# Kernel optimization log

Measured on AMD Instinct MI355X. Metric: run time of the kernel, lower is better.

Reference implementation:

```python
import jax, jax.numpy as jnp
import numpy as np

HEADS = 2
K_HOP = 2
RATIO = 0.8
NEG_SLOPE = 0.01


def seg_softmax(logits, seg, num_seg):
    # torch_geometric.utils.softmax: numerically stable segment softmax
    m = jax.ops.segment_max(logits, seg, num_segments=num_seg)
    e = jnp.exp(logits - m[seg])
    d = jax.ops.segment_sum(e, seg, num_segments=num_seg)
    return e / d[seg]


def _attention(key_value, query, seg, num_seg, Wk, W1, W2, W3):
    # Attention.forward with enable_BN=False; weights stored [in,out] so x@W == torch Linear
    a = key_value @ Wk
    h = jnp.concatenate([a, query, a - query, a * query], axis=-1)  # [N,4H]
    h = jax.nn.leaky_relu(h @ W1, NEG_SLOPE)
    h = jax.nn.leaky_relu(h @ W2, NEG_SLOPE)
    h = jax.nn.leaky_relu(h @ W3, NEG_SLOPE)  # [N,1]
    return seg_softmax(h[:, 0], seg, num_seg)[:, None]  # att_weights [N,1]


def setup_inputs():
    key = jax.random.key(0)
    ks = jax.random.split(key, 10)
    B, n, H, epg = 64, 64, 128, 2048
    N = B * n
    x = jax.random.normal(ks[0], (N, H), jnp.float32)
    src = jax.random.randint(ks[1], (B, epg), 0, n)
    dst = jax.random.randint(ks[2], (B, epg), 0, n)
    off = (jnp.arange(B) * n)[:, None]
    edge_index = jnp.stack([(src + off).reshape(-1), (dst + off).reshape(-1)], 0)
    edge_weight = jax.random.uniform(ks[3], (B * epg,), jnp.float32)
    target_x = jax.random.normal(ks[4], (B, H), jnp.float32)
    batch_ixs = jnp.repeat(jnp.arange(B), n)
    s = lambda i, sh: jax.random.normal(ks[i], sh, jnp.float32) / np.sqrt(sh[-2])
    # index 0=cluster_att, 1=query_att, 2=cluster_att2, 3=query_att2
    att_Wk = s(5, (4, H, H))
    att_W1 = s(6, (4, 4 * H, 2 * H))
    att_W2 = s(7, (4, 2 * H, H))
    att_W3 = s(8, (4, H, 1))
    lin_W = s(9, (HEADS, H, H))
    return dict(x=x, edge_index=edge_index, edge_weight=edge_weight, target_x=target_x,
                batch_ixs=batch_ixs, att_Wk=att_Wk, att_W1=att_W1, att_W2=att_W2,
                att_W3=att_W3, lin_W=lin_W)


def reference(x, edge_index, edge_weight, target_x, batch_ixs, att_Wk, att_W1, att_W2, att_W3, lin_W):
    N, H = x.shape
    B = target_x.shape[0]
    n = N // B
    # ---- gcn_norm with self loops (fill 1.0) ----
    loop = jnp.arange(N)
    row = jnp.concatenate([edge_index[0], loop])
    col = jnp.concatenate([edge_index[1], loop])
    w = jnp.concatenate([edge_weight, jnp.ones((N,), edge_weight.dtype)])
    deg = jax.ops.segment_sum(w, col, num_segments=N)
    dinv = jnp.where(deg > 0, jax.lax.rsqrt(jnp.maximum(deg, 1e-12)), 0.0)
    ew = dinv[row] * w * dinv[col]  # [L]
    # ---- k-hop propagation ----
    def hop(v):
        return jax.ops.segment_sum(v[row] * ew[:, None], col, num_segments=N)
    x_q = x
    for _ in range(K_HOP):
        x_q = hop(x_q)
    qt = target_x[batch_ixs]  # repeat_interleave by per-graph counts (sorted batch)
    # ---- multi-head edge attention (reuse_att_w=True, dropout=0 -> E identical per head) ----
    f1 = _attention(x, x_q, batch_ixs, B, att_Wk[0], att_W1[0], att_W2[0], att_W3[0])
    f2 = _attention(x, qt, batch_ixs, B, att_Wk[1], att_W1[1], att_W2[1], att_W3[1])
    E = jax.nn.leaky_relu(f1[col] + f2[row], NEG_SLOPE)  # [L,1]
    E = seg_softmax(E[:, 0], col, N)[:, None]
    x_c = jnp.zeros_like(x)
    E_g = jnp.zeros((row.shape[0], 1), x.dtype)
    agg = jax.ops.segment_sum(x[row] * E, col, num_segments=N)
    for h in range(HEADS):
        x_c = x_c + jax.nn.leaky_relu(x + agg @ lin_W[h], NEG_SLOPE)
        E_g = E_g + E
    x_c = x_c / HEADS
    E_g = E_g / HEADS
    # ---- second k-hop + cluster scoring ----
    x_q2 = x_c
    for _ in range(K_HOP):
        x_q2 = hop(x_q2)
    g1 = _attention(x_c, x_q2, batch_ixs, B, att_Wk[2], att_W1[2], att_W2[2], att_W3[2])
    g2 = _attention(x_c, qt, batch_ixs, B, att_Wk[3], att_W1[3], att_W2[3], att_W3[3])
    # stack over heads then mean == g1+g2 (same attention modules reused per head)
    cluster_score = seg_softmax((g1 + g2)[:, 0], batch_ixs, B)  # [N]
    # ---- per-graph topk (ratio) ----
    kk = int(np.ceil(RATIO * n))
    _, idx = jax.lax.top_k(cluster_score.reshape(B, n), kk)  # descending, matches PyG topk
    perm = (idx + (jnp.arange(B) * n)[:, None]).reshape(-1)  # [Nk]
    x_out = x[perm] * cluster_score[perm][:, None]
    batch_out = batch_ixs[perm]
    # ---- S^T A S (dense equivalent of SparseTensor triple product) ----
    A_d = jnp.zeros((N, N), x.dtype).at[row, col].add(ew)
    S_d = jnp.zeros((N, N), x.dtype).at[row, col].add(E_g[:, 0])
    S_p = S_d[:, perm]  # S[:, perm] -> [N, Nk]
    A2 = S_p.T @ (A_d @ S_p)  # [Nk, Nk]
    Nk = perm.shape[0]
    A2 = A2.at[jnp.arange(Nk), jnp.arange(Nk)].set(1.0)  # fill_diag(1.0)
    return x_out, A2, batch_out, perm
```

## Files before the change

### kernel.cpp

```cpp
#include <hip/hip_runtime.h>

#define KK 52
#define NKOUT 3328
#define NEG 0.01f

typedef __attribute__((ext_vector_type(8))) __bf16 bf16x8;
typedef __attribute__((ext_vector_type(16))) float floatx16;

__device__ __forceinline__ float lrelu(float v){ return v > 0.f ? v : NEG*v; }

#define SW(r, ko) ((r)*40 + ((ko) ^ ((((r)>>3)&3) << 3)))

__device__ __forceinline__ void split_store8(const float* vv, __bf16* P0, __bf16* P1, __bf16* P2, int addr){
  bf16x8 p1, p2, p3;
  #pragma unroll
  for (int j = 0; j < 8; j++){
    __bf16 b1 = (__bf16)vv[j];
    float r1 = vv[j] - (float)b1;
    __bf16 b2 = (__bf16)r1;
    float r2 = r1 - (float)b2;
    p1[j] = b1; p2[j] = b2; p3[j] = (__bf16)r2;
  }
  *(bf16x8*)(P0 + addr) = p1;
  *(bf16x8*)(P1 + addr) = p2;
  *(bf16x8*)(P2 + addr) = p3;
}

__device__ __forceinline__ void mfma6(const __bf16* A0, const __bf16* A1, const __bf16* A2,
                                      const __bf16* B0, const __bf16* B1, const __bf16* B2,
                                      int aoff, int boff, floatx16* acc){
  bf16x8 a1 = *(const bf16x8*)(A0 + aoff);
  bf16x8 a2 = *(const bf16x8*)(A1 + aoff);
  bf16x8 a3 = *(const bf16x8*)(A2 + aoff);
  bf16x8 b1 = *(const bf16x8*)(B0 + boff);
  bf16x8 b2 = *(const bf16x8*)(B1 + boff);
  bf16x8 b3 = *(const bf16x8*)(B2 + boff);
  floatx16 c = *acc;
  c = __builtin_amdgcn_mfma_f32_32x32x16_bf16(a1,b1,c,0,0,0);
  c = __builtin_amdgcn_mfma_f32_32x32x16_bf16(a1,b2,c,0,0,0);
  c = __builtin_amdgcn_mfma_f32_32x32x16_bf16(a2,b1,c,0,0,0);
  c = __builtin_amdgcn_mfma_f32_32x32x16_bf16(a1,b3,c,0,0,0);
  c = __builtin_amdgcn_mfma_f32_32x32x16_bf16(a3,b1,c,0,0,0);
  c = __builtin_amdgcn_mfma_f32_32x32x16_bf16(a2,b2,c,0,0,0);
  *acc = c;
}

__device__ __forceinline__ void g_gemm(const float* __restrict__ A0, int ldA,
                                       const float* __restrict__ W0, int ldW, int K,
                                       __bf16* pb, floatx16* oA, floatx16* oB){
  __bf16 *As0 = pb, *As1 = pb+2560, *As2 = pb+5120;
  __bf16 *Bs0 = pb+7680, *Bs1 = pb+12800, *Bs2 = pb+17920;
  int tid = threadIdx.x;
  int sar = tid >> 2, sako = (tid & 3)*8;
  int bn = tid & 127, bk = (tid >> 7)*16;
  int wv_ = tid >> 6, L = tid & 63, m = L & 31, half = L >> 5;
  int rA = 32*(wv_ & 1) + m, rB0 = (wv_ >> 1)*32 + m, rB1 = rB0 + 64;
  const float* arow = A0 + (size_t)sar*ldA;
  floatx16 accA, accB;
  #pragma unroll
  for (int i = 0; i < 16; i++){ accA[i] = 0.f; accB[i] = 0.f; }
  float ra[8], wv[16];
  {
    float4 v0 = *(const float4*)(arow + sako);
    float4 v1 = *(const float4*)(arow + sako + 4);
    ra[0]=v0.x; ra[1]=v0.y; ra[2]=v0.z; ra[3]=v0.w; ra[4]=v1.x; ra[5]=v1.y; ra[6]=v1.z; ra[7]=v1.w;
    #pragma unroll
    for (int j = 0; j < 16; j++) wv[j] = W0[(size_t)(bk + j)*ldW + bn];
  }
  for (int k0 = 0; k0 < K; k0 += 32){
    split_store8(ra, As0, As1, As2, SW(sar, sako));
    split_store8(wv,     Bs0, Bs1, Bs2, SW(bn, bk));
    split_store8(wv + 8, Bs0, Bs1, Bs2, SW(bn, bk + 8));
    __syncthreads();
    int k1 = k0 + 32;
    float ra2[8], wv2[16];
    if (k1 < K){
      float4 v0 = *(const float4*)(arow + k1 + sako);
      float4 v1 = *(const float4*)(arow + k1 + sako + 4);
      ra2[0]=v0.x; ra2[1]=v0.y; ra2[2]=v0.z; ra2[3]=v0.w; ra2[4]=v1.x; ra2[5]=v1.y; ra2[6]=v1.z; ra2[7]=v1.w;
      #pragma unroll
      for (int j = 0; j < 16; j++) wv2[j] = W0[(size_t)(k1 + bk + j)*ldW + bn];
    }
    #pragma unroll
    for (int kg = 0; kg < 2; kg++){
      int ko = kg*16 + half*8;
      mfma6(As0,As1,As2, Bs0,Bs1,Bs2, SW(rA,ko), SW(rB0,ko), &accA);
      mfma6(As0,As1,As2, Bs0,Bs1,Bs2, SW(rA,ko), SW(rB1,ko), &accB);
    }
    __syncthreads();
    if (k1 < K){
      #pragma unroll
      for (int j = 0; j < 8; j++) ra[j] = ra2[j];
      #pragma unroll
      for (int j = 0; j < 16; j++) wv[j] = wv2[j];
    }
  }
  *oA = accA; *oB = accB;
}

__device__ __forceinline__ void g_gemm_h64(const float* __restrict__ arow, const float* __restrict__ qrow,
                                           const float* __restrict__ W1fz, int colbase,
                                           __bf16* pb, floatx16* oC){
  __bf16 *As0 = pb, *As1 = pb+2560, *As2 = pb+5120;
  __bf16 *Bs0 = pb+7680, *Bs1 = pb+10240, *Bs2 = pb+12800;
  int tid = threadIdx.x;
  int sar = tid >> 2, sako = (tid & 3)*8;
  int bn = tid & 63, bk = (tid >> 6)*8;
  int col = colbase + bn;
  int wv_ = tid >> 6, L = tid & 63, m = L & 31, half = L >> 5;
  int rA = 32*(wv_ & 1) + m, rB = 32*(wv_ >> 1) + m;
  auto loadA = [&](int k0, float* r){
    int seg = k0 >> 7, kl = (k0 & 127) + sako;
    if (seg == 0){
      float4 a0 = *(const float4*)(arow + kl), a1 = *(const float4*)(arow + kl + 4);
      r[0]=a0.x; r[1]=a0.y; r[2]=a0.z; r[3]=a0.w; r[4]=a1.x; r[5]=a1.y; r[6]=a1.z; r[7]=a1.w;
    } else if (seg == 1){
      float4 q0 = *(const float4*)(qrow + kl), q1 = *(const float4*)(qrow + kl + 4);
      r[0]=q0.x; r[1]=q0.y; r[2]=q0.z; r[3]=q0.w; r[4]=q1.x; r[5]=q1.y; r[6]=q1.z; r[7]=q1.w;
    } else {
      float4 a0 = *(const float4*)(arow + kl), a1 = *(const float4*)(arow + kl + 4);
      float4 q0 = *(const float4*)(qrow + kl), q1 = *(const float4*)(qrow + kl + 4);
      r[0]=a0.x*q0.x; r[1]=a0.y*q0.y; r[2]=a0.z*q0.z; r[3]=a0.w*q0.w;
      r[4]=a1.x*q1.x; r[5]=a1.y*q1.y; r[6]=a1.z*q1.z; r[7]=a1.w*q1.w;
    }
  };
  auto loadB = [&](int k0, float* r){
    #pragma unroll
    for (int j = 0; j < 8; j++) r[j] = W1fz[(size_t)(k0 + bk + j)*256 + col];
  };
  floatx16 acc;
  #pragma unroll
  for (int i = 0; i < 16; i++) acc[i] = 0.f;
  float ra[8], wv[8];
  loadA(0, ra); loadB(0, wv);
  for (int k0 = 0; k0 < 384; k0 += 32){
    split_store8(ra, As0, As1, As2, SW(sar, sako));
    split_store8(wv, Bs0, Bs1, Bs2, SW(bn, bk));
    __syncthreads();
    int k1 = k0 + 32;
    float ra2[8], wv2[8];
    if (k1 < 384){ loadA(k1, ra2); loadB(k1, wv2); }
    #pragma unroll
    for (int kg = 0; kg < 2; kg++){
      int ko = kg*16 + half*8;
      mfma6(As0,As1,As2, Bs0,Bs1,Bs2, SW(rA,ko), SW(rB,ko), &acc);
    }
    __syncthreads();
    if (k1 < 384){
      #pragma unroll
      for (int j = 0; j < 8; j++){ ra[j] = ra2[j]; wv[j] = wv2[j]; }
    }
  }
  *oC = acc;
}

__device__ __forceinline__ void c_write(floatx16 accA, floatx16 accB, float* C0, int ldC, int act){
  int tid = threadIdx.x, wv_ = tid >> 6, L = tid & 63, m = L & 31, half = L >> 5;
  int rB0 = (wv_ >> 1)*32 + m, rB1 = rB0 + 64;
  int row0 = 32*(wv_ & 1) + 4*half;
  #pragma unroll
  for (int reg = 0; reg < 16; reg++){
    int row = row0 + (reg & 3) + 8*(reg >> 2);
    float va = accA[reg], vb = accB[reg];
    if (act){ va = lrelu(va); vb = lrelu(vb); }
    C0[(size_t)row*ldC + rB0] = va;
    C0[(size_t)row*ldC + rB1] = vb;
  }
}

__device__ __forceinline__ void c_write64(floatx16 acc, float* C0, int ldC, int act){
  int tid = threadIdx.x, wv_ = tid >> 6, L = tid & 63, m = L & 31, half = L >> 5;
  int col = 32*(wv_ >> 1) + m;
  int row0 = 32*(wv_ & 1) + 4*half;
  #pragma unroll
  for (int reg = 0; reg < 16; reg++){
    int row = row0 + (reg & 3) + 8*(reg >> 2);
    float v = acc[reg];
    if (act) v = lrelu(v);
    C0[(size_t)row*ldC + col] = v;
  }
}

__device__ __forceinline__ void hop2_run(const float* A, const float* VfullL,
                                         const float* srcG, float* dstG,
                                         float* Vt, float* Tt){
  int tid = threadIdx.x;
  int tc = (tid & 31)*2, tf = (tid >> 5)*4;
  for (int f0 = 0; f0 < 128; f0 += 32){
    if (!VfullL){
      for (int o = tid; o < 2048; o += 256){
        int r = o >> 5, f = o & 31;
        Vt[o] = srcG[r*128 + f0 + f];
      }
      __syncthreads();
    }
    float a00,a01,a02,a03,a10,a11,a12,a13;
    a00=a01=a02=a03=a10=a11=a12=a13=0.f;
    for (int r = 0; r < 64; r++){
      float x0 = A[r*64 + tc], x1 = A[r*64 + tc + 1];
      float4 v4 = VfullL ? *(const float4*)&VfullL[r*128 + f0 + tf]
                         : *(const float4*)&Vt[r*32 + tf];
      a00 += x0*v4.x; a01 += x0*v4.y; a02 += x0*v4.z; a03 += x0*v4.w;
      a10 += x1*v4.x; a11 += x1*v4.y; a12 += x1*v4.z; a13 += x1*v4.w;
    }
    *(float4*)&Tt[tc*32 + tf]     = make_float4(a00,a01,a02,a03);
    *(float4*)&Tt[(tc+1)*32 + tf] = make_float4(a10,a11,a12,a13);
    __syncthreads();
    a00=a01=a02=a03=a10=a11=a12=a13=0.f;
    for (int r = 0; r < 64; r++){
      float x0 = A[r*64 + tc], x1 = A[r*64 + tc + 1];
      float4 v4 = *(const float4*)&Tt[r*32 + tf];
      a00 += x0*v4.x; a01 += x0*v4.y; a02 += x0*v4.z; a03 += x0*v4.w;
      a10 += x1*v4.x; a11 += x1*v4.y; a12 += x1*v4.z; a13 += x1*v4.w;
    }
    *(float4*)(dstG + tc*128 + f0 + tf)     = make_float4(a00,a01,a02,a03);
    *(float4*)(dstG + (tc+1)*128 + f0 + tf) = make_float4(a10,a11,a12,a13);
    __syncthreads();
  }
}

__global__ __launch_bounds__(256) void k_p0(const int* __restrict__ ei, const float* __restrict__ ew,
                                            const float* __restrict__ x, const float* __restrict__ Wk,
                                            const float* __restrict__ W1,
                                            float* A_g, float* M_g, float* xq, float* a_buf, float* W1f){
  __shared__ __align__(16) char POOL[57856];
  float* pf = (float*)POOL;
  __bf16* pb = (__bf16*)POOL;
  int blk = blockIdx.x, tid = threadIdx.x;
  if (blk < 64){
    int b = blk;
    float* Ws = pf; float* Mc = pf + 4096; float* dv = pf + 8192;
    for (int i = tid; i < 4096; i += 256){ Ws[i] = 0.f; Mc[i] = 0.f; }
    __syncthreads();
    const int* r0 = ei + b*2048;
    const int* c0 = ei + 64*2048 + b*2048;
    const float* w0 = ew + b*2048;
    int base = b*64;
    for (int e = tid; e < 2048; e += 256){
      int r = r0[e] - base, c = c0[e] - base;
      atomicAdd(&Ws[r*64 + c], w0[e]);
      atomicAdd(&Mc[r*64 + c], 1.f);
    }
    if (tid < 64){ atomicAdd(&Ws[tid*65], 1.f); atomicAdd(&Mc[tid*65], 1.f); }
    __syncthreads();
    if (tid < 64){
      float d = 0.f;
      for (int r = 0; r < 64; r++) d += Ws[r*64 + tid];
      dv[tid] = d > 0.f ? rsqrtf(fmaxf(d, 1e-12f)) : 0.f;
    }
    __syncthreads();
    for (int i = tid; i < 4096; i += 256){
      int r = i >> 6, c = i & 63;
      float a = dv[r]*Ws[i]*dv[c];
      Ws[i] = a;
      A_g[b*4096 + i] = a;
      M_g[b*4096 + i] = Mc[i];
    }
    __syncthreads();
    hop2_run(Ws, nullptr, x + (size_t)b*8192, xq + (size_t)b*8192, pf + 8256, pf + 10304);
  } else if (blk < 192){
    int idx = blk - 64, z = idx >> 6, b = idx & 63;
    floatx16 cA, cB;
    g_gemm(x + (size_t)b*8192, 128, Wk + (size_t)z*16384, 128, 128, pb, &cA, &cB);
    c_write(cA, cB, a_buf + (size_t)z*524288 + (size_t)b*8192, 128, 0);
  } else {
    int idx0 = (blk - 192)*6144;
    for (int i = tid; i < 6144; i += 256){
      int g = idx0 + i;
      int zz = g / 98304;
      int r = g - zz*98304;
      int kr = r >> 8, c = r & 255;
      const float* Wz = W1 + (size_t)zz*131072;
      float v;
      if (kr < 128)       v = Wz[kr*256 + c] + Wz[(kr + 256)*256 + c];
      else if (kr < 256)  v = Wz[kr*256 + c] - Wz[(kr + 128)*256 + c];
      else                v = Wz[(kr + 128)*256 + c];
      W1f[g] = v;
    }
  }
}

__global__ __launch_bounds__(256) void k_h1(const float* __restrict__ a_buf, const float* __restrict__ q0,
                                            const float* __restrict__ tgt, const float* __restrict__ W1fp,
                                            float* h1){
  __shared__ __align__(16) char POOL[30720];
  __bf16* pb = (__bf16*)POOL;
  int blk = blockIdx.x, tid = threadIdx.x;
  int b = blk >> 3, z = (blk >> 2) & 1, nq = blk & 3;
  int sar = tid >> 2;
  const float* arow = a_buf + (size_t)z*524288 + ((size_t)b*64 + sar)*128;
  const float* qrow = z ? (tgt + (size_t)b*128) : (q0 + ((size_t)b*64 + sar)*128);
  floatx16 c;
  g_gemm_h64(arow, qrow, W1fp + (size_t)z*98304, nq*64, pb, &c);
  c_write64(c, h1 + (size_t)z*1048576 + (size_t)b*16384 + nq*64, 256, 1);
}

__global__ __launch_bounds__(256) void k_w2(const float* __restrict__ h1, const float* __restrict__ W2,
                                            const float* __restrict__ W3, float* outF){
  __shared__ __align__(16) char POOL[46720];
  float* pf = (float*)POOL;
  __bf16* pb = (__bf16*)POOL;
  int blk = blockIdx.x, tid = threadIdx.x;
  int z = blk >> 6, b = blk & 63;
  const float* W2z = W2 + (size_t)z*32768;
  const float* W3z = W3 + z*128;
  floatx16 cA, cB;
  g_gemm(h1 + (size_t)z*1048576 + (size_t)b*64*256, 256, W2z, 128, 256, pb, &cA, &cB);
  int wv_ = tid >> 6, L = tid & 63, m = L & 31, half = L >> 5;
  int rB0 = (wv_ >> 1)*32 + m, rB1 = rB0 + 64;
  float wA = W3z[rB0], wB = W3z[rB1];
  float* lgp = pf + 11520;
  float c[16];
  #pragma unroll
  for (int reg = 0; reg < 16; reg++) c[reg] = lrelu(cA[reg])*wA + lrelu(cB[reg])*wB;
  #pragma unroll
  for (int off = 1; off < 32; off <<= 1)
    #pragma unroll
    for (int reg = 0; reg < 16; reg++) c[reg] += __shfl_xor(c[reg], off);
  if (m == 0){
    #pragma unroll
    for (int reg = 0; reg < 16; reg++) lgp[wv_*32 + half*16 + reg] = c[reg];
  }
  __syncthreads();
  if (tid < 64){
    int row = tid, wva = row >> 5, rem = row & 31;
    int hf = (rem >> 2) & 1, rg = (rem & 3) + 4*(rem >> 3);
    float l = lrelu(lgp[wva*32 + hf*16 + rg] + lgp[(wva + 2)*32 + hf*16 + rg]);
    float mx = l;
    #pragma unroll
    for (int off = 32; off; off >>= 1) mx = fmaxf(mx, __shfl_xor(mx, off));
    float e = expf(l - mx);
    float s = e;
    #pragma unroll
    for (int off = 32; off; off >>= 1) s += __shfl_xor(s, off);
    outF[z*4096 + b*64 + row] = e/s;
  }
}

__global__ __launch_bounds__(256) void k_edge(const float* __restrict__ M_g, const float* __restrict__ fb,
                                              const float* __restrict__ x, float* __restrict__ S_g,
                                              float* __restrict__ agg){
  __shared__ __align__(16) float Mc[4096];
  __shared__ __align__(16) float xb[8192];
  __shared__ float f1s[64], f2s[64];
  int b = blockIdx.x, tid = threadIdx.x;
  for (int i = tid; i < 4096; i += 256) Mc[i] = M_g[b*4096 + i];
  for (int i = tid*4; i < 8192; i += 1024)
    *(float4*)&xb[i] = *(const float4*)(x + (size_t)b*8192 + i);
  if (tid < 64) f1s[tid] = fb[b*64 + tid];
  else if (tid < 128) f2s[tid - 64] = fb[4096 + b*64 + (tid - 64)];
  __syncthreads();
  int c = tid >> 2, sub = tid & 3;
  float m = -1e30f;
  for (int r = sub; r < 64; r += 4)
    if (Mc[r*64 + c] > 0.f) m = fmaxf(m, lrelu(f1s[c] + f2s[r]));
  m = fmaxf(m, __shfl_xor(m, 1));
  m = fmaxf(m, __shfl_xor(m, 2));
  float s = 0.f;
  for (int r = sub; r < 64; r += 4){
    float mc = Mc[r*64 + c];
    if (mc > 0.f) s += mc*expf(lrelu(f1s[c] + f2s[r]) - m);
  }
  s += __shfl_xor(s, 1);
  s += __shfl_xor(s, 2);
  for (int r = sub; r < 64; r += 4){
    float mc = Mc[r*64 + c];
    float v = 0.f;
    if (mc > 0.f) v = mc*expf(lrelu(f1s[c] + f2s[r]) - m)/s;
    Mc[r*64 + c] = v;
  }
  __syncthreads();
  for (int i = tid; i < 4096; i += 256) S_g[b*4096 + i] = Mc[i];
  int tc = (tid & 15)*4, tf = (tid >> 4)*8;
  float acc[4][8];
  #pragma unroll
  for (int i = 0; i < 4; i++)
    #pragma unroll
    for (int j = 0; j < 8; j++) acc[i][j] = 0.f;
  for (int r = 0; r < 64; r++){
    float4 e4 = *(const float4*)&Mc[r*64 + tc];
    float4 x0 = *(const float4*)&xb[r*128 + tf];
    float4 x1 = *(const float4*)&xb[r*128 + tf + 4];
    float e_[4] = {e4.x,e4.y,e4.z,e4.w};
    float x_[8] = {x0.x,x0.y,x0.z,x0.w,x1.x,x1.y,x1.z,x1.w};
    #pragma unroll
    for (int ci = 0; ci < 4; ci++)
      #pragma unroll
      for (int fj = 0; fj < 8; fj++) acc[ci][fj] += e_[ci]*x_[fj];
  }
  #pragma unroll
  for (int ci = 0; ci < 4; ci++){
    *(float4*)(agg + (size_t)b*8192 + (tc+ci)*128 + tf)     = make_float4(acc[ci][0],acc[ci][1],acc[ci][2],acc[ci][3]);
    *(float4*)(agg + (size_t)b*8192 + (tc+ci)*128 + tf + 4) = make_float4(acc[ci][4],acc[ci][5],acc[ci][6],acc[ci][7]);
  }
}

__global__ __launch_bounds__(256) void k_linxchop(const float* __restrict__ aggb, const float* __restrict__ x,
                                                  const float* __restrict__ linW, const float* __restrict__ A_g,
                                                  float* xcb, float* xq2){
  __shared__ __align__(16) char POOL[57856];
  float* pf = (float*)POOL;
  __bf16* pb = (__bf16*)POOL;
  int b = blockIdx.x, tid = threadIdx.x;
  floatx16 h0A, h0B, h1A, h1B2;
  g_gemm(aggb + (size_t)b*8192, 128, linW, 128, 128, pb, &h0A, &h0B);
  g_gemm(aggb + (size_t)b*8192, 128, linW + 16384, 128, 128, pb, &h1A, &h1B2);
  float* xcV = pf; float* Ab = pf + 8192; float* Tt = pf + 12288;
  {
    int wv_ = tid >> 6, L = tid & 63, m = L & 31, half = L >> 5;
    int rB0 = (wv_ >> 1)*32 + m, rB1 = rB0 + 64, row0 = 32*(wv_ & 1) + 4*half;
    #pragma unroll
    for (int reg = 0; reg < 16; reg++){
      int row = row0 + (reg & 3) + 8*(reg >> 2);
      float xv0 = x[((size_t)b*64 + row)*128 + rB0];
      float v0 = 0.5f*(lrelu(xv0 + h0A[reg]) + lrelu(xv0 + h1A[reg]));
      xcV[row*128 + rB0] = v0;
      xcb[(size_t)b*8192 + row*128 + rB0] = v0;
      float xv1 = x[((size_t)b*64 + row)*128 + rB1];
      float v1 = 0.5f*(lrelu(xv1 + h0B[reg]) + lrelu(xv1 + h1B2[reg]));
      xcV[row*128 + rB1] = v1;
      xcb[(size_t)b*8192 + row*128 + rB1] = v1;
    }
  }
  for (int i = tid*4; i < 4096; i += 1024)
    *(float4*)&Ab[i] = *(const float4*)(A_g + b*4096 + i);
  __syncthreads();
  hop2_run(Ab, xcV, nullptr, xq2 + (size_t)b*8192, Tt, Tt);
}

__global__ __launch_bounds__(256) void k_wkg(const float* __restrict__ xcb, const float* __restrict__ Wkg,
                                             float* a_buf){
  __shared__ __align__(16) char POOL[46080];
  __bf16* pb = (__bf16*)POOL;
  int blk = blockIdx.x;
  int z = blk >> 6, b = blk & 63;
  floatx16 cA, cB;
  g_gemm(xcb + (size_t)b*8192, 128, Wkg + (size_t)z*16384, 128, 128, pb, &cA, &cB);
  c_write(cA, cB, a_buf + (size_t)z*524288 + (size_t)b*8192, 128, 0);
}

__global__ __launch_bounds__(256) void k_A2c(const float* __restrict__ gb, const float* __restrict__ x,
                                             const float* __restrict__ A_g, const float* __restrict__ S_g,
                                             float* C2g, float* outX, float* outB, float* outP){
  __shared__ __align__(16) float At[64*68];
  __shared__ __align__(16) float Sp[64*56];
  __shared__ __align__(16) float Tq[64*56];
  __shared__ int pi[64];
  __shared__ float pv[64];
  int b = blockIdx.x, tid = threadIdx.x;
  if (tid < 64){
    int lane = tid;
    float l = gb[b*64 + lane] + gb[4096 + b*64 + lane];
    float m = l;
    #pragma unroll
    for (int off = 32; off; off >>= 1) m = fmaxf(m, __shfl_xor(m, off));
    float e = expf(l - m);
    float sm = e;
    #pragma unroll
    for (int off = 32; off; off >>= 1) sm += __shfl_xor(sm, off);
    float v = e/sm;
    int idx = lane;
    #pragma unroll
    for (int k = 2; k <= 64; k <<= 1){
      #pragma unroll
      for (int j = k >> 1; j > 0; j >>= 1){
        float ov = __shfl_xor(v, j);
        int   oi = __shfl_xor(idx, j);
        bool ascBlock = (lane & k) == 0;
        bool iAmLow   = (lane & j) == 0;
        bool otherPrec = (ov > v) || (ov == v && oi < idx);
        bool take = (ascBlock == iAmLow) ? otherPrec : !otherPrec;
        if (take){ v = ov; idx = oi; }
      }
    }
    pi[lane] = idx; pv[lane] = v;
    if (lane < KK){
      outB[b*KK + lane] = (float)b;
      outP[b*KK + lane] = (float)(b*64 + idx);
    }
  }
  __syncthreads();
  for (int o = tid*4; o < KK*128; o += 1024){
    int j = o >> 7, f = o & 127;
    float4 xv = *(const float4*)(x + ((size_t)b*64 + pi[j])*128 + f);
    float sv = pv[j];
    *(float4*)(outX + (size_t)b*KK*128 + o) = make_float4(xv.x*sv, xv.y*sv, xv.z*sv, xv.w*sv);
  }
  for (int idx = tid; idx < 4096; idx += 256){
    int i = idx >> 6, k = idx & 63;
    At[k*68 + i] = A_g[b*4096 + idx];
  }
  for (int idx = tid; idx < 4096; idx += 256){
    int k = idx >> 6, t = idx & 63;
    if (t < 56) Sp[k*56 + t] = (t < KK) ? S_g[b*4096 + k*64 + pi[t]] : 0.f;
  }
  __syncthreads();
  if (tid < 224){
    int i0 = (tid/14)*4, t0 = (tid % 14)*4;
    float acc[4][4];
    #pragma unroll
    for (int a = 0; a < 4; a++)
      #pragma unroll
      for (int c = 0; c < 4; c++) acc[a][c] = 0.f;
    for (int k = 0; k < 64; k++){
      float4 a4 = *(const float4*)&At[k*68 + i0];
      float4 s4 = *(const float4*)&Sp[k*56 + t0];
      float a_[4] = {a4.x,a4.y,a4.z,a4.w};
      float s_[4] = {s4.x,s4.y,s4.z,s4.w};
      #pragma unroll
      for (int ii = 0; ii < 4; ii++)
        #pragma unroll
        for (int tt = 0; tt < 4; tt++) acc[ii][tt] += a_[ii]*s_[tt];
    }
    #pragma unroll
    for (int ii = 0; ii < 4; ii++)
      *(float4*)&Tq[(i0+ii)*56 + t0] = make_float4(acc[ii][0],acc[ii][1],acc[ii][2],acc[ii][3]);
  }
  __syncthreads();
  if (tid < 169){
    int a0 = (tid/13)*4, t0 = (tid % 13)*4;
    float acc[4][4];
    #pragma unroll
    for (int a = 0; a < 4; a++)
      #pragma unroll
      for (int c = 0; c < 4; c++) acc[a][c] = 0.f;
    for (int i = 0; i < 64; i++){
      float4 s4 = *(const float4*)&Sp[i*56 + a0];
      float4 t4 = *(const float4*)&Tq[i*56 + t0];
      float s_[4] = {s4.x,s4.y,s4.z,s4.w};
      float t_[4] = {t4.x,t4.y,t4.z,t4.w};
      #pragma unroll
      for (int aa = 0; aa < 4; aa++)
        #pragma unroll
        for (int tt = 0; tt < 4; tt++) acc[aa][tt] += s_[aa]*t_[tt];
    }
    #pragma unroll
    for (int aa = 0; aa < 4; aa++)
      #pragma unroll
      for (int tt = 0; tt < 4; tt++){
        int a = a0 + aa, t = t0 + tt;
        C2g[b*(KK*KK) + a*KK + t] = (a == t) ? 1.f : acc[aa][tt];
      }
  }
}

__global__ __launch_bounds__(256) void k_A2w(const float* __restrict__ C2g, float* __restrict__ outA2){
  int g = blockIdx.x*256 + threadIdx.x;
  int row = g/832, c4 = g - row*832;
  int b = row/KK, al = row - b*KK;
  int rel = c4 - b*13;
  float4 val;
  if (rel >= 0 && rel < 13){
    val = *(const float4*)(C2g + (size_t)b*(KK*KK) + al*KK + rel*4);
  } else {
    val = make_float4(0.f, 0.f, 0.f, 0.f);
  }
  *(float4*)(outA2 + (size_t)g*4) = val;
}

extern "C" void kernel_launch(void* const* d_in, const int* in_sizes, int n_in,
                              void* d_out, int out_size, void* d_ws, size_t ws_size,
                              hipStream_t stream){
  const float* x    = (const float*)d_in[0];
  const int*   ei   = (const int*)d_in[1];
  const float* ew   = (const float*)d_in[2];
  const float* tgt  = (const float*)d_in[3];
  const float* Wk   = (const float*)d_in[5];
  const float* W1   = (const float*)d_in[6];
  const float* W2   = (const float*)d_in[7];
  const float* W3   = (const float*)d_in[8];
  const float* linW = (const float*)d_in[9];
  float* out = (float*)d_out;

  float* wf   = (float*)d_ws;
  float* A_g  = wf;
  float* M_g  = wf + 262144;
  float* S_g  = wf + 524288;
  float* xq   = wf + 786432;
  float* xq2  = wf + 1310720;
  float* aggb = wf + 1835008;
  float* xcb  = wf + 2359296;
  float* a_buf= wf + 2883584;
  float* h1   = wf + 3932160;
  float* fb   = wf + 6029312;
  float* gb   = wf + 6037504;
  float* W1f  = wf + 6045696;
  float* C2g  = wf + 6438912;

  float* outX  = out;
  float* outA2 = out + 425984;
  float* outB  = out + 425984 + 11075584;
  float* outP  = outB + NKOUT;

  k_p0<<<dim3(256), dim3(256), 0, stream>>>(ei, ew, x, Wk, W1, A_g, M_g, xq, a_buf, W1f);
  k_h1<<<dim3(512), dim3(256), 0, stream>>>(a_buf, xq, tgt, W1f, h1);
  k_w2<<<dim3(128), dim3(256), 0, stream>>>(h1, W2, W3, fb);
  k_edge<<<dim3(64), dim3(256), 0, stream>>>(M_g, fb, x, S_g, aggb);
  k_linxchop<<<dim3(64), dim3(256), 0, stream>>>(aggb, x, linW, A_g, xcb, xq2);
  k_wkg<<<dim3(128), dim3(256), 0, stream>>>(xcb, Wk + 2*16384, a_buf);
  k_h1<<<dim3(512), dim3(256), 0, stream>>>(a_buf, xq2, tgt, W1f + 2*98304, h1);
  k_w2<<<dim3(128), dim3(256), 0, stream>>>(h1, W2 + 2*32768, W3 + 2*128, gb);
  k_A2c<<<dim3(64), dim3(256), 0, stream>>>(gb, x, A_g, S_g, C2g, outX, outB, outP);
  k_A2w<<<dim3(10816), dim3(256), 0, stream>>>(C2g, outA2);
}
```

Measured before the change: 257.5 us.

## Split W2/Wk GEMMs into 64-column halves, zero A2 early, write diagonal blocks directly

The W2 and Wk-gather GEMMs now use a 64-column tile variant with twice as many blocks, so more CUs are busy. The W2 stage writes partial logits per column half, and the leaky-relu plus segment softmax move into the consumer kernels. The large dense A2 output is zeroed by extra blocks appended to the first kernel, and the per-graph A2 blocks are written straight into place. This removes the separate 10816-block copy kernel and the intermediate C2 buffer, at the cost of recomputing the softmax in two consumers.

```diff
diff --git a/kernel.cpp b/kernel.cpp
--- a/kernel.cpp
+++ b/kernel.cpp
@@ -96,6 +96,55 @@
     }
   }
   *oA = accA; *oB = accB;
+}
+
+__device__ __forceinline__ void g_gemm64(const float* __restrict__ A0, int ldA,
+                                         const float* __restrict__ W0, int ldW, int K,
+                                         __bf16* pb, floatx16* oC){
+  __bf16 *As0 = pb, *As1 = pb+2560, *As2 = pb+5120;
+  __bf16 *Bs0 = pb+7680, *Bs1 = pb+10240, *Bs2 = pb+12800;
+  int tid = threadIdx.x;
+  int sar = tid >> 2, sako = (tid & 3)*8;
+  int bn = tid & 63, bk = (tid >> 6)*8;
+  int wv_ = tid >> 6, L = tid & 63, m = L & 31, half = L >> 5;
+  int rA = 32*(wv_ & 1) + m, rB = 32*(wv_ >> 1) + m;
+  const float* arow = A0 + (size_t)sar*ldA;
+  floatx16 acc;
+  #pragma unroll
+  for (int i = 0; i < 16; i++) acc[i] = 0.f;
+  float ra[8], wv[8];
+  {
+    float4 v0 = *(const float4*)(arow + sako);
+    float4 v1 = *(const float4*)(arow + sako + 4);
+    ra[0]=v0.x; ra[1]=v0.y; ra[2]=v0.z; ra[3]=v0.w; ra[4]=v1.x; ra[5]=v1.y; ra[6]=v1.z; ra[7]=v1.w;
+    #pragma unroll
+    for (int j = 0; j < 8; j++) wv[j] = W0[(size_t)(bk + j)*ldW + bn];
+  }
+  for (int k0 = 0; k0 < K; k0 += 32){
+    split_store8(ra, As0, As1, As2, SW(sar, sako));
+    split_store8(wv, Bs0, Bs1, Bs2, SW(bn, bk));
+    __syncthreads();
+    int k1 = k0 + 32;
+    float ra2[8], wv2[8];
+    if (k1 < K){
+      float4 v0 = *(const float4*)(arow + k1 + sako);
+      float4 v1 = *(const float4*)(arow + k1 + sako + 4);
+      ra2[0]=v0.x; ra2[1]=v0.y; ra2[2]=v0.z; ra2[3]=v0.w; ra2[4]=v1.x; ra2[5]=v1.y; ra2[6]=v1.z; ra2[7]=v1.w;
+      #pragma unroll
+      for (int j = 0; j < 8; j++) wv2[j] = W0[(size_t)(k1 + bk + j)*ldW + bn];
+    }
+    #pragma unroll
+    for (int kg = 0; kg < 2; kg++){
+      int ko = kg*16 + half*8;
+      mfma6(As0,As1,As2, Bs0,Bs1,Bs2, SW(rA,ko), SW(rB,ko), &acc);
+    }
+    __syncthreads();
+    if (k1 < K){
+      #pragma unroll
+      for (int j = 0; j < 8; j++){ ra[j] = ra2[j]; wv[j] = wv2[j]; }
+    }
+  }
+  *oC = acc;
 }
 
 __device__ __forceinline__ void g_gemm_h64(const float* __restrict__ arow, const float* __restrict__ qrow,
@@ -222,7 +271,8 @@
 __global__ __launch_bounds__(256) void k_p0(const int* __restrict__ ei, const float* __restrict__ ew,
                                             const float* __restrict__ x, const float* __restrict__ Wk,
                                             const float* __restrict__ W1,
-                                            float* A_g, float* M_g, float* xq, float* a_buf, float* W1f){
+                                            float* A_g, float* M_g, float* xq, float* a_buf, float* W1f,
+                                            float* outA2){
   __shared__ __align__(16) char POOL[57856];
   float* pf = (float*)POOL;
   __bf16* pb = (__bf16*)POOL;
@@ -263,7 +313,7 @@
     floatx16 cA, cB;
     g_gemm(x + (size_t)b*8192, 128, Wk + (size_t)z*16384, 128, 128, pb, &cA, &cB);
     c_write(cA, cB, a_buf + (size_t)z*524288 + (size_t)b*8192, 128, 0);
-  } else {
+  } else if (blk < 256){
     int idx0 = (blk - 192)*6144;
     for (int i = tid; i < 6144; i += 256){
       int g = idx0 + i;
@@ -277,6 +327,11 @@
       else                v = Wz[(kr + 128)*256 + c];
       W1f[g] = v;
     }
+  } else {
+    float4* p = (float4*)outA2;
+    int base = (blk - 256)*1024 + tid;
+    #pragma unroll
+    for (int i = 0; i < 4; i++) p[base + i*256] = make_float4(0.f,0.f,0.f,0.f);
   }
 }
 
@@ -295,49 +350,40 @@
   c_write64(c, h1 + (size_t)z*1048576 + (size_t)b*16384 + nq*64, 256, 1);
 }
 
-__global__ __launch_bounds__(256) void k_w2(const float* __restrict__ h1, const float* __restrict__ W2,
-                                            const float* __restrict__ W3, float* outF){
-  __shared__ __align__(16) char POOL[46720];
-  float* pf = (float*)POOL;
+__global__ __launch_bounds__(256) void k_w2p(const float* __restrict__ h1, const float* __restrict__ W2,
+                                             const float* __restrict__ W3, float* __restrict__ lp){
+  __shared__ __align__(16) char POOL[30720];
+  __shared__ float lgp[128];
   __bf16* pb = (__bf16*)POOL;
   int blk = blockIdx.x, tid = threadIdx.x;
-  int z = blk >> 6, b = blk & 63;
-  const float* W2z = W2 + (size_t)z*32768;
-  const float* W3z = W3 + z*128;
-  floatx16 cA, cB;
-  g_gemm(h1 + (size_t)z*1048576 + (size_t)b*64*256, 256, W2z, 128, 256, pb, &cA, &cB);
+  int b = blk >> 2, z = (blk >> 1) & 1, nh = blk & 1;
+  floatx16 c;
+  g_gemm64(h1 + (size_t)z*1048576 + (size_t)b*16384, 256,
+           W2 + (size_t)z*32768 + nh*64, 128, 256, pb, &c);
   int wv_ = tid >> 6, L = tid & 63, m = L & 31, half = L >> 5;
-  int rB0 = (wv_ >> 1)*32 + m, rB1 = rB0 + 64;
-  float wA = W3z[rB0], wB = W3z[rB1];
-  float* lgp = pf + 11520;
-  float c[16];
-  #pragma unroll
-  for (int reg = 0; reg < 16; reg++) c[reg] = lrelu(cA[reg])*wA + lrelu(cB[reg])*wB;
+  int col = 32*(wv_ >> 1) + m;
+  float w = W3[z*128 + nh*64 + col];
+  float v[16];
+  #pragma unroll
+  for (int reg = 0; reg < 16; reg++) v[reg] = lrelu(c[reg])*w;
   #pragma unroll
   for (int off = 1; off < 32; off <<= 1)
     #pragma unroll
-    for (int reg = 0; reg < 16; reg++) c[reg] += __shfl_xor(c[reg], off);
+    for (int reg = 0; reg < 16; reg++) v[reg] += __shfl_xor(v[reg], off);
   if (m == 0){
     #pragma unroll
-    for (int reg = 0; reg < 16; reg++) lgp[wv_*32 + half*16 + reg] = c[reg];
+    for (int reg = 0; reg < 16; reg++) lgp[wv_*32 + half*16 + reg] = v[reg];
   }
   __syncthreads();
   if (tid < 64){
-    int row = tid, wva = row >> 5, rem = row & 31;
+    int row = tid, rh = row >> 5, rem = row & 31;
     int hf = (rem >> 2) & 1, rg = (rem & 3) + 4*(rem >> 3);
-    float l = lrelu(lgp[wva*32 + hf*16 + rg] + lgp[(wva + 2)*32 + hf*16 + rg]);
-    float mx = l;
-    #pragma unroll
-    for (int off = 32; off; off >>= 1) mx = fmaxf(mx, __shfl_xor(mx, off));
-    float e = expf(l - mx);
-    float s = e;
-    #pragma unroll
-    for (int off = 32; off; off >>= 1) s += __shfl_xor(s, off);
-    outF[z*4096 + b*64 + row] = e/s;
-  }
-}
-
-__global__ __launch_bounds__(256) void k_edge(const float* __restrict__ M_g, const float* __restrict__ fb,
+    float p = lgp[rh*32 + hf*16 + rg] + lgp[(rh + 2)*32 + hf*16 + rg];
+    lp[(z*2 + nh)*4096 + b*64 + row] = p;
+  }
+}
+
+__global__ __launch_bounds__(256) void k_edge(const float* __restrict__ M_g, const float* __restrict__ lp,
                                               const float* __restrict__ x, float* __restrict__ S_g,
                                               float* __restrict__ agg){
   __shared__ __align__(16) float Mc[4096];
@@ -347,8 +393,19 @@
   for (int i = tid; i < 4096; i += 256) Mc[i] = M_g[b*4096 + i];
   for (int i = tid*4; i < 8192; i += 1024)
     *(float4*)&xb[i] = *(const float4*)(x + (size_t)b*8192 + i);
-  if (tid < 64) f1s[tid] = fb[b*64 + tid];
-  else if (tid < 128) f2s[tid - 64] = fb[4096 + b*64 + (tid - 64)];
+  if (tid < 128){
+    int z = tid >> 6, r = tid & 63;
+    float d = lp[(z*2)*4096 + b*64 + r] + lp[(z*2 + 1)*4096 + b*64 + r];
+    float l = lrelu(d);
+    float mx = l;
+    #pragma unroll
+    for (int off = 32; off; off >>= 1) mx = fmaxf(mx, __shfl_xor(mx, off));
+    float e = expf(l - mx);
+    float s = e;
+    #pragma unroll
+    for (int off = 32; off; off >>= 1) s += __shfl_xor(s, off);
+    (z ? f2s : f1s)[r] = e/s;
+  }
   __syncthreads();
   int c = tid >> 2, sub = tid & 3;
   float m = -1e30f;
@@ -430,18 +487,18 @@
 
 __global__ __launch_bounds__(256) void k_wkg(const float* __restrict__ xcb, const float* __restrict__ Wkg,
                                              float* a_buf){
-  __shared__ __align__(16) char POOL[46080];
+  __shared__ __align__(16) char POOL[30720];
   __bf16* pb = (__bf16*)POOL;
   int blk = blockIdx.x;
-  int z = blk >> 6, b = blk & 63;
-  floatx16 cA, cB;
-  g_gemm(xcb + (size_t)b*8192, 128, Wkg + (size_t)z*16384, 128, 128, pb, &cA, &cB);
-  c_write(cA, cB, a_buf + (size_t)z*524288 + (size_t)b*8192, 128, 0);
-}
-
-__global__ __launch_bounds__(256) void k_A2c(const float* __restrict__ gb, const float* __restrict__ x,
+  int b = blk >> 2, z = (blk >> 1) & 1, nh = blk & 1;
+  floatx16 c;
+  g_gemm64(xcb + (size_t)b*8192, 128, Wkg + (size_t)z*16384 + nh*64, 128, 128, pb, &c);
+  c_write64(c, a_buf + (size_t)z*524288 + (size_t)b*8192 + nh*64, 128, 0);
+}
+
+__global__ __launch_bounds__(256) void k_A2c(const float* __restrict__ lp, const float* __restrict__ x,
                                              const float* __restrict__ A_g, const float* __restrict__ S_g,
-                                             float* C2g, float* outX, float* outB, float* outP){
+                                             float* outA2, float* outX, float* outB, float* outP){
   __shared__ __align__(16) float At[64*68];
   __shared__ __align__(16) float Sp[64*56];
   __shared__ __align__(16) float Tq[64*56];
@@ -450,7 +507,21 @@
   int b = blockIdx.x, tid = threadIdx.x;
   if (tid < 64){
     int lane = tid;
-    float l = gb[b*64 + lane] + gb[4096 + b*64 + lane];
+    float f[2];
+    #pragma unroll
+    for (int z = 0; z < 2; z++){
+      float d = lp[(z*2)*4096 + b*64 + lane] + lp[(z*2 + 1)*4096 + b*64 + lane];
+      float l = lrelu(d);
+      float mx = l;
+      #pragma unroll
+      for (int off = 32; off; off >>= 1) mx = fmaxf(mx, __shfl_xor(mx, off));
+      float e = expf(l - mx);
+      float sm = e;
+      #pragma unroll
+      for (int off = 32; off; off >>= 1) sm += __shfl_xor(sm, off);
+      f[z] = e/sm;
+    }
+    float l = f[0] + f[1];
     float m = l;
     #pragma unroll
     for (int off = 32; off; off >>= 1) m = fmaxf(m, __shfl_xor(m, off));
@@ -535,27 +606,16 @@
         for (int tt = 0; tt < 4; tt++) acc[aa][tt] += s_[aa]*t_[tt];
     }
     #pragma unroll
-    for (int aa = 0; aa < 4; aa++)
-      #pragma unroll
-      for (int tt = 0; tt < 4; tt++){
-        int a = a0 + aa, t = t0 + tt;
-        C2g[b*(KK*KK) + a*KK + t] = (a == t) ? 1.f : acc[aa][tt];
-      }
-  }
-}
-
-__global__ __launch_bounds__(256) void k_A2w(const float* __restrict__ C2g, float* __restrict__ outA2){
-  int g = blockIdx.x*256 + threadIdx.x;
-  int row = g/832, c4 = g - row*832;
-  int b = row/KK, al = row - b*KK;
-  int rel = c4 - b*13;
-  float4 val;
-  if (rel >= 0 && rel < 13){
-    val = *(const float4*)(C2g + (size_t)b*(KK*KK) + al*KK + rel*4);
-  } else {
-    val = make_float4(0.f, 0.f, 0.f, 0.f);
-  }
-  *(float4*)(outA2 + (size_t)g*4) = val;
+    for (int aa = 0; aa < 4; aa++){
+      int a = a0 + aa;
+      float4 o;
+      o.x = (a == t0    ) ? 1.f : acc[aa][0];
+      o.y = (a == t0 + 1) ? 1.f : acc[aa][1];
+      o.z = (a == t0 + 2) ? 1.f : acc[aa][2];
+      o.w = (a == t0 + 3) ? 1.f : acc[aa][3];
+      *(float4*)(outA2 + (size_t)(b*KK + a)*NKOUT + b*KK + t0) = o;
+    }
+  }
 }
 
 extern "C" void kernel_launch(void* const* d_in, const int* in_sizes, int n_in,
@@ -582,24 +642,21 @@
   float* xcb  = wf + 2359296;
   float* a_buf= wf + 2883584;
   float* h1   = wf + 3932160;
-  float* fb   = wf + 6029312;
-  float* gb   = wf + 6037504;
+  float* lp   = wf + 6029312;
   float* W1f  = wf + 6045696;
-  float* C2g  = wf + 6438912;
 
   float* outX  = out;
   float* outA2 = out + 425984;
   float* outB  = out + 425984 + 11075584;
   float* outP  = outB + NKOUT;
 
-  k_p0<<<dim3(256), dim3(256), 0, stream>>>(ei, ew, x, Wk, W1, A_g, M_g, xq, a_buf, W1f);
+  k_p0<<<dim3(2960), dim3(256), 0, stream>>>(ei, ew, x, Wk, W1, A_g, M_g, xq, a_buf, W1f, outA2);
   k_h1<<<dim3(512), dim3(256), 0, stream>>>(a_buf, xq, tgt, W1f, h1);
-  k_w2<<<dim3(128), dim3(256), 0, stream>>>(h1, W2, W3, fb);
-  k_edge<<<dim3(64), dim3(256), 0, stream>>>(M_g, fb, x, S_g, aggb);
+  k_w2p<<<dim3(256), dim3(256), 0, stream>>>(h1, W2, W3, lp);
+  k_edge<<<dim3(64), dim3(256), 0, stream>>>(M_g, lp, x, S_g, aggb);
   k_linxchop<<<dim3(64), dim3(256), 0, stream>>>(aggb, x, linW, A_g, xcb, xq2);
-  k_wkg<<<dim3(128), dim3(256), 0, stream>>>(xcb, Wk + 2*16384, a_buf);
+  k_wkg<<<dim3(256), dim3(256), 0, stream>>>(xcb, Wk + 2*16384, a_buf);
   k_h1<<<dim3(512), dim3(256), 0, stream>>>(a_buf, xq2, tgt, W1f + 2*98304, h1);
-  k_w2<<<dim3(128), dim3(256), 0, stream>>>(h1, W2 + 2*32768, W3 + 2*128, gb);
-  k_A2c<<<dim3(64), dim3(256), 0, stream>>>(gb, x, A_g, S_g, C2g, outX, outB, outP);
-  k_A2w<<<dim3(10816), dim3(256), 0, stream>>>(C2g, outA2);
-}
+  k_w2p<<<dim3(256), dim3(256), 0, stream>>>(h1, W2 + 2*32768, W3 + 2*128, lp);
+  k_A2c<<<dim3(64), dim3(256), 0, stream>>>(lp, x, A_g, S_g, outA2, outX, outB, outP);
+}
```

Result: faster. 241.3 us (-6.3%).
